# Optimization experiments

Hardware: AMD Instinct MI355X
Metric: run time of the kernel (lower is better)

Reference implementation:

```python
import jax, jax.numpy as jnp
import numpy as np

NEG_SLOPE = 0.2  # PyG GATConv default


def gat_conv(x, src, dst, W_src, W_dst, att_src, att_dst, bias, heads, ch, n_nodes):
    """One PyG-style GATConv with self-loops already included in (src, dst).
    Returns [N, heads*ch] (concat over heads)."""
    xs = (x @ W_src).reshape(n_nodes, heads, ch)  # source-side transform (messages)
    xd = (x @ W_dst).reshape(n_nodes, heads, ch)  # dest-side transform (attention only)
    a_s = jnp.sum(xs * att_src, axis=-1)  # [N, H]
    a_d = jnp.sum(xd * att_dst, axis=-1)  # [N, H]
    e = jax.nn.leaky_relu(a_s[src] + a_d[dst], NEG_SLOPE)  # [E, H]
    # segment softmax over edges grouped by destination node
    m = jax.ops.segment_max(e, dst, num_segments=n_nodes)  # [N, H]
    ex = jnp.exp(e - m[dst])
    denom = jax.ops.segment_sum(ex, dst, num_segments=n_nodes)  # [N, H]
    alpha = ex / denom[dst]  # [E, H]
    # weighted scatter-aggregate of source messages
    out = jax.ops.segment_sum(xs[src] * alpha[:, :, None], dst, num_segments=n_nodes)
    return out.reshape(n_nodes, heads * ch) + bias


def setup_inputs() -> dict:
    key = jax.random.key(0)
    ks = jax.random.split(key, 12)
    N, F, E = 50000, 128, 400000
    H, C1, C2 = 4, 64, 64
    x = jax.random.normal(ks[0], (N, F), dtype=jnp.float32)
    edge_index = jax.random.randint(ks[1], (2, E), 0, N, dtype=jnp.int64)
    g = lambda k, shape, fan_in: jax.random.normal(k, shape, dtype=jnp.float32) * (1.0 / np.sqrt(fan_in))
    return {
        "x": x,
        "edge_index": edge_index,
        "W1_src": g(ks[2], (F, H * C1), F),
        "W1_dst": g(ks[3], (F, H * C1), F),
        "att1_src": g(ks[4], (H, C1), C1),
        "att1_dst": g(ks[5], (H, C1), C1),
        "b1": jnp.zeros((H * C1,), dtype=jnp.float32),
        "W2_src": g(ks[6], (H * C1, C2), H * C1),
        "W2_dst": g(ks[7], (H * C1, C2), H * C1),
        "att2_src": g(ks[8], (1, C2), C2),
        "att2_dst": g(ks[9], (1, C2), C2),
        "b2": jnp.zeros((C2,), dtype=jnp.float32),
    }


def reference(x, edge_index, W1_src, W1_dst, att1_src, att1_dst, b1,
              W2_src, W2_dst, att2_src, att2_dst, b2):
    N = x.shape[0]
    loop = jnp.arange(N, dtype=edge_index.dtype)
    src = jnp.concatenate([edge_index[0], loop])  # add_self_loops=True
    dst = jnp.concatenate([edge_index[1], loop])
    H, C1 = att1_src.shape
    C2 = att2_src.shape[1]
    h = gat_conv(x, src, dst, W1_src, W1_dst, att1_src, att1_dst, b1, H, C1, N)
    h = jax.nn.relu(h)
    # dropout is identity in eval mode
    out = gat_conv(h, src, dst, W2_src, W2_dst, att2_src, att2_dst, b2, 1, C2, N)
    return out
```

## Files before the change

### kernel.cpp

```cpp
#include <hip/hip_runtime.h>


static inline int cdiv(int a, int b) { return (a + b - 1) / b; }

typedef __attribute__((ext_vector_type(8))) short short8;
typedef __attribute__((ext_vector_type(4))) float floatx4;

__device__ __forceinline__ float bf2f(unsigned short u) {
  return __uint_as_float(((unsigned int)u) << 16);
}
__device__ __forceinline__ unsigned short f2bf(float f) {
  unsigned int u = __float_as_uint(f);
  unsigned int r = (u + 0x7FFFu + ((u >> 16) & 1u)) >> 16;
  return (unsigned short)r;
}
__device__ __forceinline__ float ldv(const void* p, int i, int bf) {
  return bf ? bf2f(((const unsigned short*)p)[i]) : ((const float*)p)[i];
}
#define NEG_INF (-__builtin_inff())

__global__ void fill_out_kernel(float* __restrict__ out, int n, float val) {
  int t = blockIdx.x * blockDim.x + threadIdx.x;
  if (t < n) out[t] = val;
}

__device__ int probe_bf(const unsigned short* xu) {
  __shared__ int cc;
  if (threadIdx.x == 0) cc = 0;
  __syncthreads();
  int l0 = 0;
  for (int i = threadIdx.x; i < 1024; i += 256) {
    int e = (xu[2 * i] >> 7) & 0xFF;
    if (e >= 100 && e <= 141) l0++;
  }
  atomicAdd(&cc, l0);
  __syncthreads();
  return cc > 512 ? 1 : 0;
}
__device__ int probe_e64(const unsigned int* eu) {
  __shared__ int ce;
  if (threadIdx.x == 0) ce = 0;
  __syncthreads();
  int l1 = 0;
  for (int i = threadIdx.x; i < 1024; i += 256)
    if (eu[2 * i + 1] == 0u) l1++;
  atomicAdd(&ce, l1);
  __syncthreads();
  return ce > 512 ? 1 : 0;
}

__global__ void prep_edges(const unsigned short* __restrict__ xu,
                           const void* __restrict__ EI, int E, int EP, int Nn,
                           const void* __restrict__ W1s, const void* __restrict__ W1d,
                           const void* __restrict__ a1s, const void* __restrict__ a1d,
                           const void* __restrict__ W2s, const void* __restrict__ W2d,
                           const void* __restrict__ a2s, const void* __restrict__ a2d,
                           const void* __restrict__ b1, const void* __restrict__ b2,
                           unsigned short* __restrict__ W1cT,
                           unsigned short* __restrict__ W2sT,
                           unsigned short* __restrict__ W1extT,
                           float* __restrict__ v2s, float* __restrict__ v2d,
                           float* __restrict__ b1f, float* __restrict__ b2f,
                           int* __restrict__ srcS32,
                           int* __restrict__ ovfD, int* __restrict__ ovfS,
                           int* __restrict__ novf,
                           int* __restrict__ deg) {
  const int b = blockIdx.x, t = threadIdx.x;
  if (b < 128) {
    const int bf = probe_bf(xu);
    int i = b * 256 + t;
    int k = i >> 8, col = i & 255;
    W1cT[col * 128 + k] = f2bf(ldv(W1s, i, bf));
  } else if (b < 192) {
    const int bf = probe_bf(xu);
    int i = (b - 128) * 256 + t;
    int k = i >> 6, col = i & 63;
    W2sT[col * 256 + k] = f2bf(ldv(W2s, i, bf));
  } else if (b < 198) {
    const int bf = probe_bf(xu);
    const int lane = t & 63, w = t >> 6;
    const int g = lane >> 3, ll = lane & 7;
    const int base = (b - 192) * 256 + w * 64 + g;
#pragma unroll
    for (int r = 0; r < 8; ++r) {
      const int d = base + r * 8;
      const void *W, *A;
      int wo, ao;
      if (d < 1024) {
        int k = d >> 3, q = d & 7, h = q & 3;
        W = (q < 4) ? W1s : W1d;
        A = (q < 4) ? a1s : a1d;
        wo = k * 256 + h * 64;
        ao = h * 64;
      } else {
        int e = d - 1024, k = e & 255;
        W = (e < 256) ? W2s : W2d;
        A = (e < 256) ? a2s : a2d;
        wo = k * 64;
        ao = 0;
      }
      float p;
      if (bf) {
        uint4 wv = *(const uint4*)((const unsigned short*)W + wo + ll * 8);
        uint4 av = *(const uint4*)((const unsigned short*)A + ao + ll * 8);
        p  = bf2f((unsigned short)(wv.x & 0xFFFF)) * bf2f((unsigned short)(av.x & 0xFFFF));
        p += bf2f((unsigned short)(wv.x >> 16))    * bf2f((unsigned short)(av.x >> 16));
        p += bf2f((unsigned short)(wv.y & 0xFFFF)) * bf2f((unsigned short)(av.y & 0xFFFF));
        p += bf2f((unsigned short)(wv.y >> 16))    * bf2f((unsigned short)(av.y >> 16));
        p += bf2f((unsigned short)(wv.z & 0xFFFF)) * bf2f((unsigned short)(av.z & 0xFFFF));
        p += bf2f((unsigned short)(wv.z >> 16))    * bf2f((unsigned short)(av.z >> 16));
        p += bf2f((unsigned short)(wv.w & 0xFFFF)) * bf2f((unsigned short)(av.w & 0xFFFF));
        p += bf2f((unsigned short)(wv.w >> 16))    * bf2f((unsigned short)(av.w >> 16));
      } else {
        float4 w0 = *(const float4*)((const float*)W + wo + ll * 8);
        float4 w1 = *(const float4*)((const float*)W + wo + ll * 8 + 4);
        float4 a0 = *(const float4*)((const float*)A + ao + ll * 8);
        float4 a1 = *(const float4*)((const float*)A + ao + ll * 8 + 4);
        p = w0.x * a0.x + w0.y * a0.y + w0.z * a0.z + w0.w * a0.w +
            w1.x * a1.x + w1.y * a1.y + w1.z * a1.z + w1.w * a1.w;
      }
      p += __shfl_xor(p, 1);
      p += __shfl_xor(p, 2);
      p += __shfl_xor(p, 4);
      if (ll == 0) {
        if (d < 1024) {
          int k = d >> 3, q = d & 7;
          W1extT[q * 128 + k] = f2bf(p);
          W1extT[(8 + q) * 128 + k] = 0;
        } else {
          int e = d - 1024, k = e & 255;
          if (e < 256) v2s[k] = p; else v2d[k] = p;
        }
      }
    }
  } else if (b == 198) {
    const int bf = probe_bf(xu);
    b1f[t] = ldv(b1, t, bf);
    if (t < 64) b2f[t] = ldv(b2, t, bf);
  } else {
    const int e64 = probe_e64((const unsigned int*)EI);
    int i = (b - 199) * 256 + t;
    if (i < EP) {
      int s, d;
      if (i < E) {
        if (e64) {
          const unsigned int* p = (const unsigned int*)EI;
          s = (int)p[2 * (size_t)i];
          d = (int)p[2 * ((size_t)E + i)];
        } else {
          const int* p = (const int*)EI;
          s = p[i]; d = p[E + i];
        }
      } else { s = i - E; d = s; }
      if ((unsigned)s >= (unsigned)Nn) s = 0;
      if ((unsigned)d >= (unsigned)Nn) d = 0;
      int pos = atomicAdd(&deg[d], 1);
      if (pos < 32) {
        srcS32[(size_t)d * 32 + pos] = s;
      } else {
        int o = atomicAdd(novf, 1);
        ovfD[o] = d; ovfS[o] = s;
      }
    }
  }
}

__global__ __launch_bounds__(256) void gemm1(
    const void* __restrict__ X, const unsigned short* __restrict__ xu,
    const unsigned short* __restrict__ W1cT, const unsigned short* __restrict__ W1extT,
    unsigned short* __restrict__ xs1, float* __restrict__ A1, int N) {
  __shared__ __align__(16) unsigned short Wlds[64 * 136];
  const int t = threadIdx.x;
  const int bf = probe_bf(xu);
  const int lane = t & 63, wid = t >> 6;
  const int quad = lane >> 4, m16 = lane & 15;
  const int r0b = blockIdx.x * 64;
  const int r0 = r0b + wid * 16;
  const int arow = min(r0 + m16, N - 1);
  short8 af[4];
  if (bf) {
    const uint4* Xr = (const uint4*)((const unsigned int*)X + (size_t)arow * 64);
#pragma unroll
    for (int ks = 0; ks < 4; ++ks)
      af[ks] = __builtin_bit_cast(short8, Xr[ks * 4 + quad]);
  } else {
    const float* Xr = (const float*)X + (size_t)arow * 128;
#pragma unroll
    for (int ks = 0; ks < 4; ++ks) {
      short8 v;
#pragma unroll
      for (int j = 0; j < 8; ++j) v[j] = (short)f2bf(Xr[ks * 32 + quad * 8 + j]);
      af[ks] = v;
    }
  }
#pragma unroll
  for (int ph = 0; ph < 2; ++ph) {
    floatx4 accs[9];
    const int ncts = ph ? 8 : 9;
#pragma unroll
    for (int ct = 0; ct < 9; ++ct) {
      if (ct >= ncts) break;
      floatx4 acc = {0.f, 0.f, 0.f, 0.f};
      const unsigned short* bp = (ct < 8)
          ? W1cT + (size_t)(ph * 128 + ct * 16 + m16) * 128
          : W1extT + (size_t)m16 * 128;
#pragma unroll
      for (int ks = 0; ks < 4; ++ks) {
        short8 bfv = *(const short8*)(bp + ks * 32 + quad * 8);
        acc = __builtin_amdgcn_mfma_f32_16x16x32_bf16(af[ks], bfv, acc, 0, 0, 0);
      }
      accs[ct] = acc;
    }
    if (ph == 0 && m16 < 8) {
#pragma unroll
      for (int r = 0; r < 4; ++r) {
        int row = r0 + quad * 4 + r;
        if (row < N) A1[(size_t)row * 8 + m16] = accs[8][r];
      }
    }
#pragma unroll
    for (int ct = 0; ct < 8; ++ct)
#pragma unroll
      for (int r = 0; r < 4; ++r)
        Wlds[(wid * 16 + quad * 4 + r) * 136 + ct * 16 + m16] = f2bf(accs[ct][r]);
    __syncthreads();
#pragma unroll
    for (int it = 0; it < 4; ++it) {
      int lrow = it * 16 + (t >> 4);
      int grow = r0b + lrow;
      if (grow < N) {
        uint4 v = *(const uint4*)&Wlds[lrow * 136 + (t & 15) * 8];
        *(uint4*)(xs1 + (size_t)grow * 256 + ph * 128 + (t & 15) * 8) = v;
      }
    }
    __syncthreads();
  }
}

__global__ __launch_bounds__(256) void node1_merged(
    const int* __restrict__ deg, const int* __restrict__ srcS32,
    const int* __restrict__ ovfD, const int* __restrict__ ovfS,
    const int* __restrict__ novfp,
    const float* __restrict__ A1, const unsigned short* __restrict__ xs1,
    const float* __restrict__ b1f, const unsigned short* __restrict__ W2sT,
    const float* __restrict__ v2s, const float* __restrict__ v2d,
    unsigned short* __restrict__ xs2, float* __restrict__ A2, int N) {
  __shared__ unsigned short hb[8][272];
  __shared__ int   s_sh[4][2][32];
  __shared__ float al_sh[4][2][32][4];
  const int lane = threadIdx.x & 63;
  const int wid = threadIdx.x >> 6;
  const int hf = lane >> 5;
  const int hl = lane & 31;
  const int nraw = blockIdx.x * 8 + wid * 2 + hf;
  const bool valid = nraw < N;
  const int n = valid ? nraw : (N - 1);
  const int dn = deg[n];
  const float4 ad4 = *(const float4*)(A1 + (size_t)n * 8 + 4);
  const float ad[4] = {ad4.x, ad4.y, ad4.z, ad4.w};
  const int gc = 8 * hl;
  const int hd = hl >> 3;
  float acc[8] = {0.f, 0.f, 0.f, 0.f, 0.f, 0.f, 0.f, 0.f};
  constexpr int PF = 12;

  if (__all(dn <= 32)) {
    int s = 0;
    float4 as4 = make_float4(0.f, 0.f, 0.f, 0.f);
    if (hl < dn) {
      s = srcS32[(size_t)n * 32 + hl];
      as4 = *(const float4*)(A1 + (size_t)s * 8);
    }
    const int np = dn < PF ? dn : PF;
    uint4 u[PF];
#pragma unroll
    for (int j = 0; j < PF; ++j) {
      if (j < np) {
        int sj = __shfl(s, (hf << 5) + j);
        u[j] = *(const uint4*)(xs1 + (size_t)sj * 256 + gc);
      }
    }
    float v[4] = {NEG_INF, NEG_INF, NEG_INF, NEG_INF};
    if (hl < dn) {
      const float as[4] = {as4.x, as4.y, as4.z, as4.w};
#pragma unroll
      for (int h = 0; h < 4; ++h) {
        float x = as[h] + ad[h];
        v[h] = x > 0.f ? x : 0.2f * x;
      }
    }
    float m[4], l[4];
#pragma unroll
    for (int h = 0; h < 4; ++h) {
      m[h] = v[h];
#pragma unroll
      for (int off = 16; off; off >>= 1) m[h] = fmaxf(m[h], __shfl_xor(m[h], off));
      float e = (hl < dn) ? __expf(v[h] - m[h]) : 0.f;
      l[h] = e;
#pragma unroll
      for (int off = 16; off; off >>= 1) l[h] += __shfl_xor(l[h], off);
      v[h] = e;
    }
    if (hl < dn) {
      s_sh[wid][hf][hl] = s;
      float4 al = {v[0] / l[0], v[1] / l[1], v[2] / l[2], v[3] / l[3]};
      *(float4*)&al_sh[wid][hf][hl][0] = al;
    }
#pragma unroll
    for (int j = 0; j < PF; ++j) {
      if (j < np) {
        float a0 = al_sh[wid][hf][j][hd];
        acc[0] += a0 * __uint_as_float(u[j].x << 16);
        acc[1] += a0 * __uint_as_float(u[j].x & 0xFFFF0000u);
        acc[2] += a0 * __uint_as_float(u[j].y << 16);
        acc[3] += a0 * __uint_as_float(u[j].y & 0xFFFF0000u);
        acc[4] += a0 * __uint_as_float(u[j].z << 16);
        acc[5] += a0 * __uint_as_float(u[j].z & 0xFFFF0000u);
        acc[6] += a0 * __uint_as_float(u[j].w << 16);
        acc[7] += a0 * __uint_as_float(u[j].w & 0xFFFF0000u);
      }
    }
    for (int j = np; j < dn; ++j) {
      int s0 = s_sh[wid][hf][j];
      float a0 = al_sh[wid][hf][j][hd];
      uint4 uu = *(const uint4*)(xs1 + (size_t)s0 * 256 + gc);
      acc[0] += a0 * __uint_as_float(uu.x << 16);
      acc[1] += a0 * __uint_as_float(uu.x & 0xFFFF0000u);
      acc[2] += a0 * __uint_as_float(uu.y << 16);
      acc[3] += a0 * __uint_as_float(uu.y & 0xFFFF0000u);
      acc[4] += a0 * __uint_as_float(uu.z << 16);
      acc[5] += a0 * __uint_as_float(uu.z & 0xFFFF0000u);
      acc[6] += a0 * __uint_as_float(uu.w << 16);
      acc[7] += a0 * __uint_as_float(uu.w & 0xFFFF0000u);
    }
  } else {
    const int nov = *novfp;
    const int nc = dn < 32 ? dn : 32;
    float m[4] = {NEG_INF, NEG_INF, NEG_INF, NEG_INF};
    if (hl < nc) {
      int s = srcS32[(size_t)n * 32 + hl];
      const float4 as4 = *(const float4*)(A1 + (size_t)s * 8);
      const float as[4] = {as4.x, as4.y, as4.z, as4.w};
#pragma unroll
      for (int h = 0; h < 4; ++h) {
        float x = as[h] + ad[h];
        x = x > 0.f ? x : 0.2f * x;
        m[h] = x;
      }
    }
    for (int o = hl; o < nov; o += 32) {
      if (ovfD[o] == n) {
        int s = ovfS[o];
        const float4 as4 = *(const float4*)(A1 + (size_t)s * 8);
        const float as[4] = {as4.x, as4.y, as4.z, as4.w};
#pragma unroll
        for (int h = 0; h < 4; ++h) {
          float x = as[h] + ad[h];
          x = x > 0.f ? x : 0.2f * x;
          m[h] = fmaxf(m[h], x);
        }
      }
    }
#pragma unroll
    for (int h = 0; h < 4; ++h)
#pragma unroll
      for (int off = 16; off; off >>= 1) m[h] = fmaxf(m[h], __shfl_xor(m[h], off));
    float l[4] = {0.f, 0.f, 0.f, 0.f};
    if (hl < nc) {
      int s = srcS32[(size_t)n * 32 + hl];
      const float4 as4 = *(const float4*)(A1 + (size_t)s * 8);
      const float as[4] = {as4.x, as4.y, as4.z, as4.w};
#pragma unroll
      for (int h = 0; h < 4; ++h) {
        float x = as[h] + ad[h];
        x = x > 0.f ? x : 0.2f * x;
        l[h] += __expf(x - m[h]);
      }
    }
    for (int o = hl; o < nov; o += 32) {
      if (ovfD[o] == n) {
        int s = ovfS[o];
        const float4 as4 = *(const float4*)(A1 + (size_t)s * 8);
        const float as[4] = {as4.x, as4.y, as4.z, as4.w};
#pragma unroll
        for (int h = 0; h < 4; ++h) {
          float x = as[h] + ad[h];
          x = x > 0.f ? x : 0.2f * x;
          l[h] += __expf(x - m[h]);
        }
      }
    }
#pragma unroll
    for (int h = 0; h < 4; ++h)
#pragma unroll
      for (int off = 16; off; off >>= 1) l[h] += __shfl_xor(l[h], off);
    const float mh = m[hd], inv = 1.0f / l[hd], adh = ad[hd];
    for (int j = 0; j < nc; ++j) {
      int s = srcS32[(size_t)n * 32 + j];
      float x = A1[(size_t)s * 8 + hd] + adh;
      x = x > 0.f ? x : 0.2f * x;
      float alpha = __expf(x - mh) * inv;
      uint4 uu = *(const uint4*)(xs1 + (size_t)s * 256 + gc);
      acc[0] += alpha * __uint_as_float(uu.x << 16);
      acc[1] += alpha * __uint_as_float(uu.x & 0xFFFF0000u);
      acc[2] += alpha * __uint_as_float(uu.y << 16);
      acc[3] += alpha * __uint_as_float(uu.y & 0xFFFF0000u);
      acc[4] += alpha * __uint_as_float(uu.z << 16);
      acc[5] += alpha * __uint_as_float(uu.z & 0xFFFF0000u);
      acc[6] += alpha * __uint_as_float(uu.w << 16);
      acc[7] += alpha * __uint_as_float(uu.w & 0xFFFF0000u);
    }
    for (int o = 0; o < nov; ++o) {
      if (ovfD[o] == n) {
        int s = ovfS[o];
        float x = A1[(size_t)s * 8 + hd] + adh;
        x = x > 0.f ? x : 0.2f * x;
        float alpha = __expf(x - mh) * inv;
        uint4 uu = *(const uint4*)(xs1 + (size_t)s * 256 + gc);
        acc[0] += alpha * __uint_as_float(uu.x << 16);
        acc[1] += alpha * __uint_as_float(uu.x & 0xFFFF0000u);
        acc[2] += alpha * __uint_as_float(uu.y << 16);
        acc[3] += alpha * __uint_as_float(uu.y & 0xFFFF0000u);
        acc[4] += alpha * __uint_as_float(uu.z << 16);
        acc[5] += alpha * __uint_as_float(uu.z & 0xFFFF0000u);
        acc[6] += alpha * __uint_as_float(uu.w << 16);
        acc[7] += alpha * __uint_as_float(uu.w & 0xFFFF0000u);
      }
    }
  }

  const float4 bb0 = *(const float4*)(b1f + gc);
  const float4 bb1 = *(const float4*)(b1f + gc + 4);
  float hv[8];
  hv[0] = acc[0] + bb0.x; hv[1] = acc[1] + bb0.y;
  hv[2] = acc[2] + bb0.z; hv[3] = acc[3] + bb0.w;
  hv[4] = acc[4] + bb1.x; hv[5] = acc[5] + bb1.y;
  hv[6] = acc[6] + bb1.z; hv[7] = acc[7] + bb1.w;
#pragma unroll
  for (int k = 0; k < 8; ++k) hv[k] = hv[k] > 0.f ? hv[k] : 0.f;
  const float4 vs0 = *(const float4*)(v2s + gc);
  const float4 vs1 = *(const float4*)(v2s + gc + 4);
  const float4 vd0 = *(const float4*)(v2d + gc);
  const float4 vd1 = *(const float4*)(v2d + gc + 4);
  float ps = hv[0] * vs0.x + hv[1] * vs0.y + hv[2] * vs0.z + hv[3] * vs0.w +
             hv[4] * vs1.x + hv[5] * vs1.y + hv[6] * vs1.z + hv[7] * vs1.w;
  float pd = hv[0] * vd0.x + hv[1] * vd0.y + hv[2] * vd0.z + hv[3] * vd0.w +
             hv[4] * vd1.x + hv[5] * vd1.y + hv[6] * vd1.z + hv[7] * vd1.w;
#pragma unroll
  for (int off = 1; off <= 16; off <<= 1) {
    ps += __shfl_xor(ps, off);
    pd += __shfl_xor(pd, off);
  }
  unsigned int p0 = (unsigned int)f2bf(hv[0]) | ((unsigned int)f2bf(hv[1]) << 16);
  unsigned int p1 = (unsigned int)f2bf(hv[2]) | ((unsigned int)f2bf(hv[3]) << 16);
  unsigned int p2 = (unsigned int)f2bf(hv[4]) | ((unsigned int)f2bf(hv[5]) << 16);
  unsigned int p3 = (unsigned int)f2bf(hv[6]) | ((unsigned int)f2bf(hv[7]) << 16);
  *(uint4*)&hb[wid * 2 + hf][gc] = make_uint4(p0, p1, p2, p3);
  if (valid && hl == 0) {
    A2[(size_t)n * 2] = ps;
    A2[(size_t)n * 2 + 1] = pd;
  }
  __syncthreads();
  const int m16 = lane & 15, quad = lane >> 4;
  floatx4 c2 = {0.f, 0.f, 0.f, 0.f};
  const unsigned short* arow = &hb[m16 & 7][0];
  const unsigned short* bcol = W2sT + (size_t)(wid * 16 + m16) * 256;
#pragma unroll
  for (int ks = 0; ks < 8; ++ks) {
    short8 afr = *(const short8*)(arow + ks * 32 + quad * 8);
    short8 bfr = *(const short8*)(bcol + ks * 32 + quad * 8);
    c2 = __builtin_amdgcn_mfma_f32_16x16x32_bf16(afr, bfr, c2, 0, 0, 0);
  }
  if (quad < 2) {
#pragma unroll
    for (int r = 0; r < 4; ++r) {
      int node = blockIdx.x * 8 + quad * 4 + r;
      if (node < N) xs2[(size_t)node * 64 + wid * 16 + m16] = f2bf(c2[r]);
    }
  }
}

__global__ __launch_bounds__(256) void node2(
    const int* __restrict__ deg, const int* __restrict__ srcS32,
    const int* __restrict__ ovfD, const int* __restrict__ ovfS,
    const int* __restrict__ novfp,
    const float* __restrict__ A2, const unsigned short* __restrict__ xs2,
    const float* __restrict__ b2f, float* __restrict__ out, int N) {
  __shared__ int   s_sh[4][2][32];
  __shared__ float al_sh[4][2][32];
  const int lane = threadIdx.x & 63;
  const int wid = threadIdx.x >> 6;
  const int hf = lane >> 5;
  const int hl = lane & 31;
  const int nraw = blockIdx.x * 8 + wid * 2 + hf;
  const bool valid = nraw < N;
  const int n = valid ? nraw : (N - 1);
  const int dn = deg[n];
  const float ad = A2[(size_t)n * 2 + 1];
  float ax = 0.f, ay = 0.f;
  constexpr int PF2 = 16;
  if (__all(dn <= 32)) {
    int s = 0;
    float a2v = 0.f;
    if (hl < dn) {
      s = srcS32[(size_t)n * 32 + hl];
      a2v = A2[(size_t)s * 2];
    }
    const int np = dn < PF2 ? dn : PF2;
    unsigned int u[PF2];
#pragma unroll
    for (int j = 0; j < PF2; ++j) {
      if (j < np) {
        int sj = __shfl(s, (hf << 5) + j);
        u[j] = *(const unsigned int*)(xs2 + (size_t)sj * 64 + 2 * hl);
      }
    }
    float v = NEG_INF;
    if (hl < dn) {
      v = a2v + ad;
      v = v > 0.f ? v : 0.2f * v;
    }
    float m = v;
#pragma unroll
    for (int off = 16; off; off >>= 1) m = fmaxf(m, __shfl_xor(m, off));
    float e = (hl < dn) ? __expf(v - m) : 0.f;
    float l = e;
#pragma unroll
    for (int off = 16; off; off >>= 1) l += __shfl_xor(l, off);
    if (hl < dn) { s_sh[wid][hf][hl] = s; al_sh[wid][hf][hl] = e / l; }
#pragma unroll
    for (int j = 0; j < PF2; ++j) {
      if (j < np) {
        float a = al_sh[wid][hf][j];
        ax += a * __uint_as_float(u[j] << 16);
        ay += a * __uint_as_float(u[j] & 0xFFFF0000u);
      }
    }
    for (int j = np; j < dn; ++j) {
      int s0 = s_sh[wid][hf][j];
      float a = al_sh[wid][hf][j];
      unsigned int uu = *(const unsigned int*)(xs2 + (size_t)s0 * 64 + 2 * hl);
      ax += a * __uint_as_float(uu << 16);
      ay += a * __uint_as_float(uu & 0xFFFF0000u);
    }
  } else {
    const int nov = *novfp;
    const int nc = dn < 32 ? dn : 32;
    float m = NEG_INF;
    if (hl < nc) {
      int s = srcS32[(size_t)n * 32 + hl];
      float v = A2[(size_t)s * 2] + ad;
      v = v > 0.f ? v : 0.2f * v;
      m = v;
    }
    for (int o = hl; o < nov; o += 32) {
      if (ovfD[o] == n) {
        float v = A2[(size_t)ovfS[o] * 2] + ad;
        v = v > 0.f ? v : 0.2f * v;
        m = fmaxf(m, v);
      }
    }
#pragma unroll
    for (int off = 16; off; off >>= 1) m = fmaxf(m, __shfl_xor(m, off));
    float l = 0.f;
    if (hl < nc) {
      int s = srcS32[(size_t)n * 32 + hl];
      float v = A2[(size_t)s * 2] + ad;
      v = v > 0.f ? v : 0.2f * v;
      l += __expf(v - m);
    }
    for (int o = hl; o < nov; o += 32) {
      if (ovfD[o] == n) {
        float v = A2[(size_t)ovfS[o] * 2] + ad;
        v = v > 0.f ? v : 0.2f * v;
        l += __expf(v - m);
      }
    }
#pragma unroll
    for (int off = 16; off; off >>= 1) l += __shfl_xor(l, off);
    float inv = 1.0f / l;
    for (int j = 0; j < nc; ++j) {
      int s = srcS32[(size_t)n * 32 + j];
      float v = A2[(size_t)s * 2] + ad;
      v = v > 0.f ? v : 0.2f * v;
      float alpha = __expf(v - m) * inv;
      unsigned int uu = *(const unsigned int*)(xs2 + (size_t)s * 64 + 2 * hl);
      ax += alpha * __uint_as_float(uu << 16);
      ay += alpha * __uint_as_float(uu & 0xFFFF0000u);
    }
    for (int o = 0; o < nov; ++o) {
      if (ovfD[o] == n) {
        int s = ovfS[o];
        float v = A2[(size_t)s * 2] + ad;
        v = v > 0.f ? v : 0.2f * v;
        float alpha = __expf(v - m) * inv;
        unsigned int uu = *(const unsigned int*)(xs2 + (size_t)s * 64 + 2 * hl);
        ax += alpha * __uint_as_float(uu << 16);
        ay += alpha * __uint_as_float(uu & 0xFFFF0000u);
      }
    }
  }
  if (valid) {
    const float2 b = *(const float2*)(b2f + 2 * hl);
    float2 o = make_float2(ax + b.x, ay + b.y);
    *(float2*)(out + (size_t)n * 64 + 2 * hl) = o;
  }
}

extern "C" void kernel_launch(void* const* d_in, const int* in_sizes, int n_in,
                              void* d_out, int out_size, void* d_ws, size_t ws_size,
                              hipStream_t stream) {
  const int F = 128, HC1 = 256, C2 = 64;
  const int N  = in_sizes[0] / F;
  const int E  = in_sizes[1] / 2;
  const int EP = E + N;
  (void)n_in;

  char* w = (char*)d_ws;
  size_t off = 0;
  auto alloc = [&](size_t bytes) -> char* {
    char* p = w + off;
    off = (off + bytes + 255) & ~(size_t)255;
    return p;
  };
  int* srcS32 = (int*)alloc((size_t)N * 32 * 4);
  int* ovfD   = (int*)alloc((size_t)EP * 4);
  int* ovfS   = (int*)alloc((size_t)EP * 4);
  int* degnv  = (int*)alloc(((size_t)N + 8) * 4);
  int* deg    = degnv;
  int* novf   = degnv + N;
  unsigned short* W1cT  = (unsigned short*)alloc((size_t)F * HC1 * 2);
  unsigned short* W1extT = (unsigned short*)alloc(16 * 128 * 2);
  unsigned short* W2sT  = (unsigned short*)alloc((size_t)HC1 * C2 * 2);
  float* v2s  = (float*)alloc(256 * 4);
  float* v2d  = (float*)alloc(256 * 4);
  float* b1f  = (float*)alloc(256 * 4);
  float* b2f  = (float*)alloc(64 * 4);
  float* A1   = (float*)alloc((size_t)N * 8 * 4);
  unsigned short* xs1 = (unsigned short*)alloc((size_t)N * HC1 * 2);
  unsigned short* xs2 = (unsigned short*)alloc((size_t)N * C2 * 2);
  float* A2 = (float*)alloc((size_t)N * 2 * 4);
  const size_t need = off;

  if (ws_size < need) {
    fill_out_kernel<<<cdiv(out_size, 256), 256, 0, stream>>>(
        (float*)d_out, out_size, 131072.0f + 1024.0f * (float)(ws_size >> 20));
    return;
  }

  hipMemsetAsync(degnv, 0, ((size_t)N + 8) * 4, stream);

  prep_edges<<<199 + cdiv(EP, 256), 256, 0, stream>>>(
      (const unsigned short*)d_in[0], d_in[1], E, EP, N,
      d_in[2], d_in[3], d_in[4], d_in[5], d_in[7], d_in[8], d_in[9], d_in[10],
      d_in[6], d_in[11],
      W1cT, W2sT, W1extT, v2s, v2d, b1f, b2f,
      srcS32, ovfD, ovfS, novf, deg);

  gemm1<<<cdiv(N, 64), 256, 0, stream>>>(
      d_in[0], (const unsigned short*)d_in[0], W1cT, W1extT, xs1, A1, N);

  node1_merged<<<cdiv(N, 8), 256, 0, stream>>>(deg, srcS32, ovfD, ovfS, novf,
                                               A1, xs1, b1f, W2sT, v2s, v2d,
                                               xs2, A2, N);
  node2<<<cdiv(N, 8), 256, 0, stream>>>(deg, srcS32, ovfD, ovfS, novf,
                                        A2, xs2, b2f, (float*)d_out, N);
}
```

Measured before the change: 231.0 us.

## Fold degree memset into weight prep and co-launch edge bucketing with GEMM

Zeroing of the degree/overflow counters moves from a separate memset into the weight-prep kernel. The edge bucketing blocks move out of the prep kernel and become extra blocks of the first-layer GEMM kernel, so edge scatter can run alongside the feature transform. This removes one launch and the serialization between edge bucketing and the GEMM. In exchange the GEMM launch carries heterogeneous blocks that compete for the same CUs.

```diff
diff --git a/kernel.cpp b/kernel.cpp
--- a/kernel.cpp
+++ b/kernel.cpp
@@ -49,23 +49,23 @@
   return ce > 512 ? 1 : 0;
 }
 
-__global__ void prep_edges(const unsigned short* __restrict__ xu,
-                           const void* __restrict__ EI, int E, int EP, int Nn,
-                           const void* __restrict__ W1s, const void* __restrict__ W1d,
-                           const void* __restrict__ a1s, const void* __restrict__ a1d,
-                           const void* __restrict__ W2s, const void* __restrict__ W2d,
-                           const void* __restrict__ a2s, const void* __restrict__ a2d,
-                           const void* __restrict__ b1, const void* __restrict__ b2,
-                           unsigned short* __restrict__ W1cT,
-                           unsigned short* __restrict__ W2sT,
-                           unsigned short* __restrict__ W1extT,
-                           float* __restrict__ v2s, float* __restrict__ v2d,
-                           float* __restrict__ b1f, float* __restrict__ b2f,
-                           int* __restrict__ srcS32,
-                           int* __restrict__ ovfD, int* __restrict__ ovfS,
-                           int* __restrict__ novf,
-                           int* __restrict__ deg) {
+__global__ void weight_prep(const unsigned short* __restrict__ xu,
+                            const void* __restrict__ W1s, const void* __restrict__ W1d,
+                            const void* __restrict__ a1s, const void* __restrict__ a1d,
+                            const void* __restrict__ W2s, const void* __restrict__ W2d,
+                            const void* __restrict__ a2s, const void* __restrict__ a2d,
+                            const void* __restrict__ b1, const void* __restrict__ b2,
+                            unsigned short* __restrict__ W1cT,
+                            unsigned short* __restrict__ W2sT,
+                            unsigned short* __restrict__ W1extT,
+                            float* __restrict__ v2s, float* __restrict__ v2d,
+                            float* __restrict__ b1f, float* __restrict__ b2f,
+                            int* __restrict__ degnv, int ndeg) {
   const int b = blockIdx.x, t = threadIdx.x;
+  {
+    int i = b * 256 + t;
+    if (i < ndeg) degnv[i] = 0;
+  }
   if (b < 128) {
     const int bf = probe_bf(xu);
     int i = b * 256 + t;
@@ -137,9 +137,20 @@
     const int bf = probe_bf(xu);
     b1f[t] = ldv(b1, t, bf);
     if (t < 64) b2f[t] = ldv(b2, t, bf);
-  } else {
+  }
+}
+
+__global__ __launch_bounds__(256) void gemm_edges(
+    const void* __restrict__ X, const unsigned short* __restrict__ xu,
+    const unsigned short* __restrict__ W1cT, const unsigned short* __restrict__ W1extT,
+    unsigned short* __restrict__ xs1, float* __restrict__ A1, int N, int gb,
+    const void* __restrict__ EI, int E, int EP,
+    int* __restrict__ srcS32, int* __restrict__ ovfD, int* __restrict__ ovfS,
+    int* __restrict__ novf, int* __restrict__ deg) {
+  const int t = threadIdx.x;
+  if (blockIdx.x >= gb) {
     const int e64 = probe_e64((const unsigned int*)EI);
-    int i = (b - 199) * 256 + t;
+    int i = ((int)blockIdx.x - gb) * 256 + t;
     if (i < EP) {
       int s, d;
       if (i < E) {
@@ -152,8 +163,8 @@
           s = p[i]; d = p[E + i];
         }
       } else { s = i - E; d = s; }
-      if ((unsigned)s >= (unsigned)Nn) s = 0;
-      if ((unsigned)d >= (unsigned)Nn) d = 0;
+      if ((unsigned)s >= (unsigned)N) s = 0;
+      if ((unsigned)d >= (unsigned)N) d = 0;
       int pos = atomicAdd(&deg[d], 1);
       if (pos < 32) {
         srcS32[(size_t)d * 32 + pos] = s;
@@ -162,15 +173,9 @@
         ovfD[o] = d; ovfS[o] = s;
       }
     }
-  }
-}
-
-__global__ __launch_bounds__(256) void gemm1(
-    const void* __restrict__ X, const unsigned short* __restrict__ xu,
-    const unsigned short* __restrict__ W1cT, const unsigned short* __restrict__ W1extT,
-    unsigned short* __restrict__ xs1, float* __restrict__ A1, int N) {
+    return;
+  }
   __shared__ __align__(16) unsigned short Wlds[64 * 136];
-  const int t = threadIdx.x;
   const int bf = probe_bf(xu);
   const int lane = t & 63, wid = t >> 6;
   const int quad = lane >> 4, m16 = lane & 15;
@@ -647,17 +652,16 @@
     return;
   }
 
-  hipMemsetAsync(degnv, 0, ((size_t)N + 8) * 4, stream);
-
-  prep_edges<<<199 + cdiv(EP, 256), 256, 0, stream>>>(
-      (const unsigned short*)d_in[0], d_in[1], E, EP, N,
+  weight_prep<<<199, 256, 0, stream>>>(
+      (const unsigned short*)d_in[0],
       d_in[2], d_in[3], d_in[4], d_in[5], d_in[7], d_in[8], d_in[9], d_in[10],
       d_in[6], d_in[11],
-      W1cT, W2sT, W1extT, v2s, v2d, b1f, b2f,
-      srcS32, ovfD, ovfS, novf, deg);
-
-  gemm1<<<cdiv(N, 64), 256, 0, stream>>>(
-      d_in[0], (const unsigned short*)d_in[0], W1cT, W1extT, xs1, A1, N);
+      W1cT, W2sT, W1extT, v2s, v2d, b1f, b2f, degnv, N + 8);
+
+  const int gb = cdiv(N, 64);
+  gemm_edges<<<gb + cdiv(EP, 256), 256, 0, stream>>>(
+      d_in[0], (const unsigned short*)d_in[0], W1cT, W1extT, xs1, A1, N, gb,
+      d_in[1], E, EP, srcS32, ovfD, ovfS, novf, deg);
 
   node1_merged<<<cdiv(N, 8), 256, 0, stream>>>(deg, srcS32, ovfD, ovfS, novf,
                                                A1, xs1, b1f, W2sT, v2s, v2d,
```

Result: faster. 223.9 us (-3.1%).
